# Optimization experiments

Hardware: AMD Instinct MI355X
Metric: run time of the kernel (lower is better)

The kernel has to match this reference:

```python
import jax, jax.numpy as jnp
import numpy as np

N = 100000        # nodes
E_RAND = 1500000  # random edges (plus N self-loops)
NFEAT = 64
NHID = 64
NHEADS = 8
ALPHA = 0.2       # leaky-relu slope


def setup_inputs() -> dict:
    key = jax.random.key(0)
    ks = jax.random.split(key, 10)
    x = jax.random.normal(ks[0], (N, NFEAT), jnp.float32)
    src = jax.random.randint(ks[1], (E_RAND,), 0, N)
    dst = jax.random.randint(ks[2], (E_RAND,), 0, N)
    loops = jnp.arange(N)
    edge_index = jnp.stack([jnp.concatenate([src, loops]),
                            jnp.concatenate([dst, loops])]).astype(jnp.int32)
    s = 0.1
    W_att = jax.random.normal(ks[3], (NHEADS, NFEAT, NHID), jnp.float32) * s
    a_att = jax.random.normal(ks[4], (NHEADS, 2 * NHID), jnp.float32) * s
    W_out = jax.random.normal(ks[5], (NHEADS * NHID, NFEAT), jnp.float32) * s
    a_out = jax.random.normal(ks[6], (2 * NFEAT,), jnp.float32) * s
    W1 = jax.random.normal(ks[7], (NFEAT, NFEAT * 10), jnp.float32) * s
    b1 = jnp.zeros((NFEAT * 10,), jnp.float32)
    W2 = jax.random.normal(ks[8], (NFEAT * 10, 10), jnp.float32) * s
    b2 = jnp.zeros((10,), jnp.float32)
    W3 = jax.random.normal(ks[9], (10, 1), jnp.float32) * s
    b3 = jnp.zeros((1,), jnp.float32)
    return dict(x=x, edge_index=edge_index, W_att=W_att, a_att=a_att,
                W_out=W_out, a_out=a_out, W1=W1, b1=b1, W2=W2, b2=b2,
                W3=W3, b3=b3)


def _gat_layer(x, row, col, W, a, concat):
    # x: [N,F], W: [F,D], a: [2D]. Faithful to pyGAT SpGraphAttentionLayer:
    # edge_e = exp(-leakyrelu(a . [h_src || h_dst])), normalized by rowsum.
    n = x.shape[0]
    h = x @ W                                   # [N, D]
    d = h.shape[1]
    alpha_src = h @ a[:d]                       # [N]
    alpha_dst = h @ a[d:]                       # [N]
    score = alpha_src[row] + alpha_dst[col]     # [E]
    edge_e = jnp.exp(-jax.nn.leaky_relu(score, ALPHA))   # [E]
    rowsum = jax.ops.segment_sum(edge_e, row, num_segments=n)            # [N]
    h_prime = jax.ops.segment_sum(edge_e[:, None] * h[col], row,
                                  num_segments=n)                        # [N, D]
    h_prime = h_prime / rowsum[:, None]
    return jax.nn.elu(h_prime) if concat else h_prime


def reference(x, edge_index, W_att, a_att, W_out, a_out, W1, b1, W2, b2, W3, b3):
    row, col = edge_index[0], edge_index[1]
    # multi-head attention, concat along features
    heads = jax.vmap(lambda W, a: _gat_layer(x, row, col, W, a, True))(W_att, a_att)  # [H,N,D]
    xh = jnp.transpose(heads, (1, 0, 2)).reshape(x.shape[0], -1)  # [N, H*D]
    xo = jax.nn.elu(_gat_layer(xh, row, col, W_out, a_out, False))  # [N, NFEAT]
    # dense MLP head
    z = jax.nn.relu(xo @ W1 + b1)
    z = jax.nn.relu(z @ W2 + b2)
    z = jax.nn.sigmoid(z @ W3 + b3)  # [N, 1]
    return z
```

## Files before the change

### kernel.cpp

```cpp
#include <hip/hip_runtime.h>
#include <hip/hip_bf16.h>
#include <math.h>

#define NF 64
#define NH 8
#define SLOPE 0.2f

typedef __hip_bfloat16 bf16;
typedef short short8 __attribute__((ext_vector_type(8)));
typedef unsigned int uint4v __attribute__((ext_vector_type(4)));
typedef float f32x4 __attribute__((ext_vector_type(4)));
typedef float f32x2 __attribute__((ext_vector_type(2)));

__device__ __forceinline__ float us2f(unsigned short u){
  union{ unsigned int i; float f; } c; c.i = ((unsigned int)u) << 16; return c.f;
}
__device__ __forceinline__ float lo16(unsigned int u){
  union{ unsigned int i; float f; } c; c.i = u << 16; return c.f;
}
__device__ __forceinline__ float hi16(unsigned int u){
  union{ unsigned int i; float f; } c; c.i = u & 0xFFFF0000u; return c.f;
}
__device__ __forceinline__ unsigned short f2b_rne(float v){
  union{ float f; unsigned int i; } c; c.f = v;
  unsigned int b = c.i + 0x7FFF + ((c.i >> 16) & 1);
  return (unsigned short)(b >> 16);
}
__device__ __forceinline__ f32x4 mfma16(short8 a, short8 b, f32x4 c){
  return __builtin_amdgcn_mfma_f32_16x16x32_bf16(a, b, c, 0, 0, 0);
}


__global__ void k_prep1(const float* __restrict__ Watt, const float* __restrict__ aatt,
                        short* __restrict__ Bp1){
  int f = blockIdx.x >> 1, ks = blockIdx.x & 1;
  int lane = threadIdx.x;
  int kg = lane >> 4, cl = lane & 15;
  int col = f * 16 + cl;
  for (int j = 0; j < 8; j++){
    int k = ks * 32 + kg * 8 + j;
    float val;
    if (col < 512){
      val = Watt[(size_t)(col >> 6) * 4096 + k * 64 + (col & 63)];
    } else {
      int h = (col - 512) & 7;
      const float* arow = aatt + h * 128 + ((col >= 520) ? 64 : 0);
      const float* wrow = Watt + (size_t)h * 4096 + k * 64;
      float s = 0.f;
      for (int d = 0; d < 64; d++) s += wrow[d] * arow[d];
      val = s;
    }
    unsigned short hu = f2b_rne(val);
    float lof = val - us2f(hu);
    Bp1[((size_t)(ks * 33) + f) * 512 + lane * 8 + j]       = (short)hu;
    Bp1[((size_t)((2 + ks) * 33) + f) * 512 + lane * 8 + j] = (short)f2b_rne(lof);
  }
}

__global__ void k_prep2(const float* __restrict__ Wout, const float* __restrict__ aout,
                        short* __restrict__ Bp2){
  int f = blockIdx.x >> 4, ks = blockIdx.x & 15;
  int lane = threadIdx.x;
  int kg = lane >> 4, cl = lane & 15;
  int col = f * 16 + cl;
  for (int j = 0; j < 8; j++){
    int k = ks * 32 + kg * 8 + j;
    float val = 0.f;
    if (col < 64){
      val = Wout[(size_t)k * 64 + col];
    } else if (col == 64 || col == 65){
      const float* arow = aout + ((col == 65) ? 64 : 0);
      const float* wrow = Wout + (size_t)k * 64;
      float s = 0.f;
      for (int d = 0; d < 64; d++) s += wrow[d] * arow[d];
      val = s;
    }
    unsigned short hu = f2b_rne(val);
    float lof = val - us2f(hu);
    Bp2[((size_t)(ks * 5) + f) * 512 + lane * 8 + j]        = (short)hu;
    Bp2[((size_t)((16 + ks) * 5) + f) * 512 + lane * 8 + j] = (short)f2b_rne(lof);
  }
}

__global__ void k_prep3(const float* __restrict__ W1, short* __restrict__ Bp3){
  int f = blockIdx.x >> 1, ks = blockIdx.x & 1;
  int lane = threadIdx.x;
  int kg = lane >> 4, cl = lane & 15;
  int col = f * 16 + cl;
  for (int j = 0; j < 8; j++){
    int k = ks * 32 + kg * 8 + j;
    float val = W1[(size_t)k * 640 + col];
    unsigned short hu = f2b_rne(val);
    float lof = val - us2f(hu);
    Bp3[((size_t)(ks * 40) + f) * 512 + lane * 8 + j]       = (short)hu;
    Bp3[((size_t)((2 + ks) * 40) + f) * 512 + lane * 8 + j] = (short)f2b_rne(lof);
  }
}

__global__ void k_prep4(const float* __restrict__ W2, short* __restrict__ Bp4){
  int ks = blockIdx.x;
  int lane = threadIdx.x;
  int kg = lane >> 4, cl = lane & 15;
  for (int j = 0; j < 8; j++){
    int k = ks * 32 + kg * 8 + j;
    float val = (cl < 10) ? W2[k * 10 + cl] : 0.f;
    unsigned short hu = f2b_rne(val);
    Bp4[((size_t)ks) * 512 + lane * 8 + j]        = (short)hu;
    Bp4[((size_t)(20 + ks)) * 512 + lane * 8 + j] = (short)f2b_rne(val - us2f(hu));
  }
}

__global__ void __launch_bounds__(256)
k_prep_x(const float* __restrict__ x, const short* __restrict__ Bp1,
         short* __restrict__ xb, float* __restrict__ a1s, float* __restrict__ a1d,
         int n_nodes){
  __shared__ short xsh[16][72];
  __shared__ short xsl[16][72];
  int n0 = blockIdx.x * 16;
  int t = threadIdx.x;
  for (int i = t; i < 16 * 64; i += 256){
    int r = i >> 6, c = i & 63;
    int nn = n0 + r;
    float v = (nn < n_nodes) ? x[(size_t)nn * NF + c] : 0.f;
    unsigned short hu = f2b_rne(v);
    float lof = v - us2f(hu);
    xsh[r][c] = (short)hu;
    xsl[r][c] = (short)f2b_rne(lof);
  }
  __syncthreads();
  for (int i = t; i < 16 * 8; i += 256){
    int r = i >> 3, c8 = (i & 7) * 8;
    int nn = n0 + r;
    if (nn < n_nodes)
      *reinterpret_cast<short8*>(xb + (size_t)nn * 64 + c8) =
        *reinterpret_cast<const short8*>(&xsh[r][c8]);
  }
  int wid = t >> 6, lane = t & 63;
  if (wid == 3){
    int rowa = lane & 15, kg = lane >> 4, cl = lane & 15;
    short8 ah[2], al[2];
    #pragma unroll
    for (int ks = 0; ks < 2; ks++){
      ah[ks] = *reinterpret_cast<const short8*>(&xsh[rowa][ks * 32 + kg * 8]);
      al[ks] = *reinterpret_cast<const short8*>(&xsl[rowa][ks * 32 + kg * 8]);
    }
    f32x4 acc = {0.f, 0.f, 0.f, 0.f};
    #pragma unroll
    for (int ks = 0; ks < 2; ks++){
      short8 b_h = *reinterpret_cast<const short8*>(Bp1 + ((size_t)(ks * 33) + 32) * 512 + lane * 8);
      short8 b_l = *reinterpret_cast<const short8*>(Bp1 + ((size_t)((2 + ks) * 33) + 32) * 512 + lane * 8);
      acc = mfma16(ah[ks], b_h, acc);
      acc = mfma16(al[ks], b_h, acc);
      acc = mfma16(ah[ks], b_l, acc);
    }
    #pragma unroll
    for (int reg = 0; reg < 4; reg++){
      int nn = n0 + kg * 4 + reg;
      if (nn < n_nodes){
        if (cl < 8) a1s[nn * NH + cl] = acc[reg];
        else        a1d[nn * NH + (cl - 8)] = acc[reg];
      }
    }
  }
}

__global__ void k_count(const int* __restrict__ row, int* __restrict__ cnt, int E){
  int e = blockIdx.x * blockDim.x + threadIdx.x;
  if (e < E) atomicAdd(&cnt[row[e]], 1);
}

__global__ void k_scan_a(const int* __restrict__ cnt, int* __restrict__ incl,
                         int* __restrict__ bsum, int n){
  __shared__ int s[1024];
  int i = blockIdx.x * 1024 + threadIdx.x;
  int v = (i < n) ? cnt[i] : 0;
  s[threadIdx.x] = v;
  __syncthreads();
  for (int d = 1; d < 1024; d <<= 1){
    int tv = (threadIdx.x >= d) ? s[threadIdx.x - d] : 0;
    __syncthreads();
    s[threadIdx.x] += tv;
    __syncthreads();
  }
  if (i < n) incl[i] = s[threadIdx.x];
  if (threadIdx.x == 1023) bsum[blockIdx.x] = s[1023];
}

__global__ void k_scan_b(const int* __restrict__ bsum, int* __restrict__ boff, int nb){
  __shared__ int s[128];
  int t = threadIdx.x;
  if (nb <= 128){
    int v = (t < nb) ? bsum[t] : 0;
    s[t] = v;
    __syncthreads();
    for (int d = 1; d < 128; d <<= 1){
      int tv = (t >= d) ? s[t - d] : 0;
      __syncthreads();
      s[t] += tv;
      __syncthreads();
    }
    if (t < nb) boff[t] = s[t] - v;
  } else if (t == 0){
    int run = 0;
    for (int b = 0; b < nb; b++){ boff[b] = run; run += bsum[b]; }
  }
}

__global__ void k_scan_c(const int* __restrict__ incl, const int* __restrict__ cnt,
                         const int* __restrict__ boff, int* __restrict__ rowptr,
                         int* __restrict__ wptr, int n){
  int i = blockIdx.x * 1024 + threadIdx.x;
  if (i < n){
    int start = incl[i] - cnt[i] + boff[blockIdx.x];
    rowptr[i] = start;
    wptr[i]   = start;
  }
}

__global__ void k_scatter(const int* __restrict__ row, const int* __restrict__ col,
                          int* __restrict__ wptr, int* __restrict__ scol, int E){
  int e = blockIdx.x * blockDim.x + threadIdx.x;
  if (e < E){
    int r = row[e];
    int pos = atomicAdd(&wptr[r], 1);
    scol[pos] = col[e];
  }
}

__global__ void __launch_bounds__(512, 2)
k_agg1_gemm2(const short* __restrict__ xb, const float* __restrict__ a1s,
             const float* __restrict__ a1d, const int* __restrict__ rowptr,
             const int* __restrict__ cnt, const int* __restrict__ scol,
             const short* __restrict__ Bp1, const short* __restrict__ Bp2,
             bf16* __restrict__ h2b, float* __restrict__ a2s,
             float* __restrict__ a2d, int n_nodes){
  __shared__ short Gh[8 * 600];
  __shared__ short xh[8][528];
  int n0   = blockIdx.x * 8;
  int wid  = threadIdx.x >> 6;
  int lane = threadIdx.x & 63;
  int h = lane >> 3, q = lane & 7;
  int n = n0 + wid;
  int gidx = wid * 600 + h * 72 + q * 8;

  if (n < n_nodes){
    float asrc = a1s[n * NH + h];
    int beg = rowptr[n], endk = beg + cnt[n];
    f32x2 acc2[4] = {{0.f,0.f},{0.f,0.f},{0.f,0.f},{0.f,0.f}};
    float rsum = 0.f;
    int k = beg;
    for (; k + 3 < endk; k += 4){
      int c0 = scol[k], c1 = scol[k + 1], c2 = scol[k + 2], c3 = scol[k + 3];
      uint4v x0 = *reinterpret_cast<const uint4v*>(xb + (size_t)c0 * 64 + q * 8);
      uint4v x1 = *reinterpret_cast<const uint4v*>(xb + (size_t)c1 * 64 + q * 8);
      uint4v x2 = *reinterpret_cast<const uint4v*>(xb + (size_t)c2 * 64 + q * 8);
      uint4v x3 = *reinterpret_cast<const uint4v*>(xb + (size_t)c3 * 64 + q * 8);
      float s0 = asrc + a1d[c0 * NH + h];
      float s1 = asrc + a1d[c1 * NH + h];
      float s2 = asrc + a1d[c2 * NH + h];
      float s3 = asrc + a1d[c3 * NH + h];
      float l0 = fmaxf(s0, SLOPE * s0);
      float l1 = fmaxf(s1, SLOPE * s1);
      float l2 = fmaxf(s2, SLOPE * s2);
      float l3 = fmaxf(s3, SLOPE * s3);
      float e0 = __expf(-l0);
      float e1 = __expf(-l1);
      float e2 = __expf(-l2);
      float e3 = __expf(-l3);
      rsum += (e0 + e1) + (e2 + e3);
      f32x2 ev0 = {e0, e0}, ev1 = {e1, e1}, ev2 = {e2, e2}, ev3 = {e3, e3};
      #pragma unroll
      for (int d = 0; d < 4; d++){
        f32x2 hv0 = {lo16(x0[d]), hi16(x0[d])};
        f32x2 hv1 = {lo16(x1[d]), hi16(x1[d])};
        f32x2 hv2 = {lo16(x2[d]), hi16(x2[d])};
        f32x2 hv3 = {lo16(x3[d]), hi16(x3[d])};
        acc2[d] += (ev0 * hv0 + ev1 * hv1) + (ev2 * hv2 + ev3 * hv3);
      }
    }
    for (; k < endk; ++k){
      int c0 = scol[k];
      uint4v x0 = *reinterpret_cast<const uint4v*>(xb + (size_t)c0 * 64 + q * 8);
      float s0 = asrc + a1d[c0 * NH + h];
      float l0 = fmaxf(s0, SLOPE * s0);
      float e0 = __expf(-l0);
      rsum += e0;
      f32x2 ev0 = {e0, e0};
      #pragma unroll
      for (int d = 0; d < 4; d++){
        f32x2 hv0 = {lo16(x0[d]), hi16(x0[d])};
        acc2[d] += ev0 * hv0;
      }
    }
    float inv = 1.f / rsum;
    short8 hv8;
    #pragma unroll
    for (int jj = 0; jj < 8; jj++)
      hv8[jj] = (short)f2b_rne(acc2[jj >> 1][jj & 1] * inv);
    *reinterpret_cast<short8*>(&Gh[gidx]) = hv8;
  } else {
    short8 z = {0,0,0,0,0,0,0,0};
    *reinterpret_cast<short8*>(&Gh[gidx]) = z;
  }
  __syncthreads();

  {
    int rowa = lane & 7;
    int kg   = lane >> 4, cl = lane & 15;
    short8 gah[2];
    #pragma unroll
    for (int ks = 0; ks < 2; ks++)
      gah[ks] = *reinterpret_cast<const short8*>(&Gh[rowa * 600 + wid * 72 + ks * 32 + kg * 8]);
    #pragma unroll
    for (int fc = 0; fc < 4; fc++){
      int f = wid * 4 + fc;
      f32x4 acc = {0.f, 0.f, 0.f, 0.f};
      #pragma unroll
      for (int ks = 0; ks < 2; ks++){
        short8 b_h = *reinterpret_cast<const short8*>(Bp1 + ((size_t)(ks * 33) + f) * 512 + lane * 8);
        short8 b_l = *reinterpret_cast<const short8*>(Bp1 + ((size_t)((2 + ks) * 33) + f) * 512 + lane * 8);
        acc = mfma16(gah[ks], b_h, acc);
        acc = mfma16(gah[ks], b_l, acc);
      }
      if (kg < 2){
        #pragma unroll
        for (int reg = 0; reg < 4; reg++){
          int r = kg * 4 + reg;
          float v = acc[reg];
          v = (v > 0.f) ? v : (__expf(v) - 1.f);
          xh[r][wid * 64 + fc * 16 + cl] = (short)f2b_rne(v);
        }
      }
    }
  }
  __syncthreads();

  if (wid < 5){
    int rowa = lane & 7;
    int kg   = lane >> 4;
    f32x4 acc = {0.f, 0.f, 0.f, 0.f};
    #pragma unroll 4
    for (int ks = 0; ks < 16; ks++){
      short8 a_h = *reinterpret_cast<const short8*>(&xh[rowa][ks * 32 + kg * 8]);
      short8 b_h = *reinterpret_cast<const short8*>(Bp2 + ((size_t)(ks * 5) + wid) * 512 + lane * 8);
      short8 b_l = *reinterpret_cast<const short8*>(Bp2 + ((size_t)((16 + ks) * 5) + wid) * 512 + lane * 8);
      acc = mfma16(a_h, b_h, acc);
      acc = mfma16(a_h, b_l, acc);
    }
    int cl = lane & 15;
    if (kg < 2){
      #pragma unroll
      for (int reg = 0; reg < 4; reg++){
        int nn = n0 + kg * 4 + reg;
        if (nn < n_nodes){
          if (wid < 4){
            h2b[(size_t)nn * 64 + wid * 16 + cl] = __float2bfloat16(acc[reg]);
          } else if (cl == 0){
            a2s[nn] = acc[reg];
          } else if (cl == 1){
            a2d[nn] = acc[reg];
          }
        }
      }
    }
  }
}

__global__ void __launch_bounds__(256)
k_agg2(const bf16* __restrict__ h2b, const float* __restrict__ a2s,
       const float* __restrict__ a2d, const int* __restrict__ rowptr,
       const int* __restrict__ cnt, const int* __restrict__ scol,
       float* __restrict__ xo, int n_nodes){
  int wid  = threadIdx.x >> 6;
  int lane = threadIdx.x & 63;
  int g = lane >> 3, sl = lane & 7;
  int n = blockIdx.x * 32 + wid * 8 + g;
  bool nv = (n < n_nodes);
  int beg = 0, deg = 0;
  float asrc = 0.f;
  if (nv){ beg = rowptr[n]; deg = cnt[n]; asrc = a2s[n]; }
  int mdeg = deg;
  #pragma unroll
  for (int m = 8; m < 64; m <<= 1){
    int o = __shfl_xor(mdeg, m);
    mdeg = (o > mdeg) ? o : mdeg;
  }
  f32x2 acc2[4] = {{0.f,0.f},{0.f,0.f},{0.f,0.f},{0.f,0.f}};
  float rsum = 0.f;
  int it = 0;
  for (; it + 1 < mdeg; it += 2){
    int i0 = (it     < deg) ? it     : 0;
    int i1 = (it + 1 < deg) ? it + 1 : 0;
    int c0 = scol[beg + i0];
    int c1 = scol[beg + i1];
    uint4v h0 = *reinterpret_cast<const uint4v*>(h2b + ((size_t)c0 << 6) + sl * 8);
    uint4v h1 = *reinterpret_cast<const uint4v*>(h2b + ((size_t)c1 << 6) + sl * 8);
    float s0 = asrc + a2d[c0];
    float s1 = asrc + a2d[c1];
    float l0 = fmaxf(s0, SLOPE * s0);
    float l1 = fmaxf(s1, SLOPE * s1);
    float e0 = __expf(-l0);
    float e1 = __expf(-l1);
    e0 = (it     < deg) ? e0 : 0.f;
    e1 = (it + 1 < deg) ? e1 : 0.f;
    rsum += e0 + e1;
    f32x2 ev0 = {e0, e0}, ev1 = {e1, e1};
    #pragma unroll
    for (int d = 0; d < 4; d++){
      f32x2 hv0 = {lo16(h0[d]), hi16(h0[d])};
      f32x2 hv1 = {lo16(h1[d]), hi16(h1[d])};
      acc2[d] += ev0 * hv0 + ev1 * hv1;
    }
  }
  if (it < mdeg){
    int i0 = (it < deg) ? it : 0;
    int c0 = scol[beg + i0];
    uint4v h0 = *reinterpret_cast<const uint4v*>(h2b + ((size_t)c0 << 6) + sl * 8);
    float s0 = asrc + a2d[c0];
    float l0 = fmaxf(s0, SLOPE * s0);
    float e0 = __expf(-l0);
    e0 = (it < deg) ? e0 : 0.f;
    rsum += e0;
    f32x2 ev0 = {e0, e0};
    #pragma unroll
    for (int d = 0; d < 4; d++){
      f32x2 hv0 = {lo16(h0[d]), hi16(h0[d])};
      acc2[d] += ev0 * hv0;
    }
  }
  if (nv){
    float inv = 1.f / rsum;
    float4 lo, hi;
    float vv[8];
    #pragma unroll
    for (int jj = 0; jj < 8; jj++){
      float v = acc2[jj >> 1][jj & 1] * inv;
      vv[jj] = (v > 0.f) ? v : (__expf(v) - 1.f);
    }
    lo.x = vv[0]; lo.y = vv[1]; lo.z = vv[2]; lo.w = vv[3];
    hi.x = vv[4]; hi.y = vv[5]; hi.z = vv[6]; hi.w = vv[7];
    *reinterpret_cast<float4*>(xo + (size_t)n * 64 + sl * 8)     = lo;
    *reinterpret_cast<float4*>(xo + (size_t)n * 64 + sl * 8 + 4) = hi;
  }
}

__global__ void __launch_bounds__(256)
k_mlp(const float* __restrict__ xo, const short* __restrict__ Bp3,
      const short* __restrict__ Bp4, const float* __restrict__ b1,
      const float* __restrict__ b2, const float* __restrict__ W3,
      const float* __restrict__ b3, float* __restrict__ out, int n_nodes){
  __shared__ short xsh[16][72];
  __shared__ short xsl[16][72];
  __shared__ short z1h[16][648];
  __shared__ float part[4][16][16];
  __shared__ float z2[16][10];
  int n0 = blockIdx.x * 16;
  int t  = threadIdx.x;
  for (int i = t; i < 16 * 64; i += 256){
    int r = i >> 6, c = i & 63;
    int nn = n0 + r;
    float v = (nn < n_nodes) ? xo[(size_t)nn * 64 + c] : 0.f;
    unsigned short hu = f2b_rne(v);
    float lof = v - us2f(hu);
    xsh[r][c] = (short)hu;
    xsl[r][c] = (short)f2b_rne(lof);
  }
  __syncthreads();
  int wid = t >> 6, lane = t & 63;
  int rowa = lane & 15, kg = lane >> 4, cl = lane & 15;
  {
    short8 ah[2], al[2];
    #pragma unroll
    for (int ks = 0; ks < 2; ks++){
      ah[ks] = *reinterpret_cast<const short8*>(&xsh[rowa][ks * 32 + kg * 8]);
      al[ks] = *reinterpret_cast<const short8*>(&xsl[rowa][ks * 32 + kg * 8]);
    }
    for (int f0 = 0; f0 < 10; f0++){
      int f = wid * 10 + f0;
      f32x4 acc = {0.f, 0.f, 0.f, 0.f};
      #pragma unroll
      for (int ks = 0; ks < 2; ks++){
        short8 b_h = *reinterpret_cast<const short8*>(Bp3 + ((size_t)(ks * 40) + f) * 512 + lane * 8);
        short8 b_l = *reinterpret_cast<const short8*>(Bp3 + ((size_t)((2 + ks) * 40) + f) * 512 + lane * 8);
        acc = mfma16(ah[ks], b_h, acc);
        acc = mfma16(al[ks], b_h, acc);
        acc = mfma16(ah[ks], b_l, acc);
      }
      int cc = f * 16 + cl;
      float bb = b1[cc];
      #pragma unroll
      for (int reg = 0; reg < 4; reg++)
        z1h[kg * 4 + reg][cc] = (short)f2b_rne(fmaxf(acc[reg] + bb, 0.f));
    }
  }
  __syncthreads();
  {
    f32x4 acc = {0.f, 0.f, 0.f, 0.f};
    #pragma unroll
    for (int kk = 0; kk < 5; kk++){
      int ks = wid * 5 + kk;
      short8 a_h = *reinterpret_cast<const short8*>(&z1h[rowa][ks * 32 + kg * 8]);
      short8 b_h = *reinterpret_cast<const short8*>(Bp4 + ((size_t)ks) * 512 + lane * 8);
      short8 b_l = *reinterpret_cast<const short8*>(Bp4 + ((size_t)(20 + ks)) * 512 + lane * 8);
      acc = mfma16(a_h, b_h, acc);
      acc = mfma16(a_h, b_l, acc);
    }
    #pragma unroll
    for (int reg = 0; reg < 4; reg++)
      part[wid][kg * 4 + reg][cl] = acc[reg];
  }
  __syncthreads();
  if (t < 160){
    int r = t / 10, c = t % 10;
    float v = (part[0][r][c] + part[1][r][c]) + (part[2][r][c] + part[3][r][c]);
    z2[r][c] = fmaxf(v + b2[c], 0.f);
  }
  __syncthreads();
  if (t < 16){
    int nn = n0 + t;
    if (nn < n_nodes){
      float acc = b3[0];
      #pragma unroll
      for (int kk = 0; kk < 10; kk++) acc += z2[t][kk] * W3[kk];
      out[nn] = 1.f / (1.f + __expf(-acc));
    }
  }
}

extern "C" void kernel_launch(void* const* d_in, const int* in_sizes, int n_in,
                              void* d_out, int out_size, void* d_ws, size_t ws_size,
                              hipStream_t stream){
  const float* x    = (const float*)d_in[0];
  const int*   ei   = (const int*)  d_in[1];
  const float* Watt = (const float*)d_in[2];
  const float* aatt = (const float*)d_in[3];
  const float* Wout = (const float*)d_in[4];
  const float* aout = (const float*)d_in[5];
  const float* W1   = (const float*)d_in[6];
  const float* b1   = (const float*)d_in[7];
  const float* W2   = (const float*)d_in[8];
  const float* b2   = (const float*)d_in[9];
  const float* W3   = (const float*)d_in[10];
  const float* b3   = (const float*)d_in[11];
  float* out = (float*)d_out;

  int N = in_sizes[0] / NF;
  int E = in_sizes[1] / 2;
  const int* row = ei;
  const int* col = ei + E;

  char* base = (char*)d_ws;
  size_t off = 0;
  auto alloc = [&](size_t bytes) -> void* {
    void* p = base + off;
    off = (off + bytes + 255) & ~(size_t)255;
    return p;
  };
  short* xb     = (short*)alloc((size_t)N * 64 * 2);
  bf16*  h2b    = (bf16*) alloc((size_t)N * 64 * 2);
  float* xo     = (float*)alloc((size_t)N * 64 * 4);
  float* a1s    = (float*)alloc((size_t)N * NH * 4);
  float* a1d    = (float*)alloc((size_t)N * NH * 4);
  float* a2s    = (float*)alloc((size_t)N * 4);
  float* a2d    = (float*)alloc((size_t)N * 4);
  int*   cnt    = (int*)  alloc((size_t)N * 4);
  int*   rowptr = (int*)  alloc((size_t)N * 4);
  int*   wptr   = (int*)  alloc((size_t)N * 4);
  int*   incl   = (int*)  alloc((size_t)N * 4);
  int    NB     = (N + 1023) / 1024;
  int*   bsum   = (int*)  alloc((size_t)NB * 4);
  int*   boff   = (int*)  alloc((size_t)NB * 4);
  int*   scol   = (int*)  alloc((size_t)E * 4);
  short* Bp1    = (short*)alloc((size_t)4 * 33 * 512 * 2);
  short* Bp2    = (short*)alloc((size_t)32 * 5 * 512 * 2);
  short* Bp3    = (short*)alloc((size_t)4 * 40 * 512 * 2);
  short* Bp4    = (short*)alloc((size_t)40 * 512 * 2);
  (void)ws_size; (void)n_in; (void)out_size;

  hipMemsetAsync(cnt, 0, (size_t)N * 4, stream);

  k_prep1     <<<66,              64, 0, stream>>>(Watt, aatt, Bp1);
  k_prep2     <<<80,              64, 0, stream>>>(Wout, aout, Bp2);
  k_prep3     <<<80,              64, 0, stream>>>(W1, Bp3);
  k_prep4     <<<20,              64, 0, stream>>>(W2, Bp4);
  k_prep_x    <<<(N + 15) / 16,  256, 0, stream>>>(x, Bp1, xb, a1s, a1d, N);
  k_count     <<<(E + 255) / 256, 256, 0, stream>>>(row, cnt, E);
  k_scan_a    <<<NB,             1024, 0, stream>>>(cnt, incl, bsum, N);
  k_scan_b    <<<1,               128, 0, stream>>>(bsum, boff, NB);
  k_scan_c    <<<NB,             1024, 0, stream>>>(incl, cnt, boff, rowptr, wptr, N);
  k_scatter   <<<(E + 255) / 256, 256, 0, stream>>>(row, col, wptr, scol, E);
  k_agg1_gemm2<<<(N + 7) / 8,     512, 0, stream>>>(xb, a1s, a1d, rowptr, cnt, scol,
                                                    Bp1, Bp2, h2b, a2s, a2d, N);
  k_agg2      <<<(N + 31) / 32,  256, 0, stream>>>(h2b, a2s, a2d, rowptr, cnt, scol, xo, N);
  k_mlp       <<<(N + 15) / 16,  256, 0, stream>>>(xo, Bp3, Bp4, b1, b2, W3, b3, out, N);
}
```

Measured before the change: 534.6 us.

## Compute first-layer edge aggregation with MFMA over 32-edge chunks

Replaces the per-lane scalar FMA edge aggregation in the fused agg1/gemm2 kernel with an MFMA formulation. Each wave handles 32 neighbours at a time: the attention weights for 8 heads become a bf16 B fragment, and gathered features form the A fragment. Partial row sums are then reduced with shuffles. This moves the aggregation arithmetic onto the matrix cores, at the cost of rounding edge weights to bf16, padding low-degree nodes to 32 edges, and doing scalar 2-byte gathers of features instead of 16-byte vector loads.

```diff
diff --git a/kernel.cpp b/kernel.cpp
--- a/kernel.cpp
+++ b/kernel.cpp
@@ -239,74 +239,72 @@
   int n0   = blockIdx.x * 8;
   int wid  = threadIdx.x >> 6;
   int lane = threadIdx.x & 63;
-  int h = lane >> 3, q = lane & 7;
+  int kg = lane >> 4, cl = lane & 15;
+  int hsel = lane & 7;
   int n = n0 + wid;
-  int gidx = wid * 600 + h * 72 + q * 8;
 
   if (n < n_nodes){
-    float asrc = a1s[n * NH + h];
-    int beg = rowptr[n], endk = beg + cnt[n];
-    f32x2 acc2[4] = {{0.f,0.f},{0.f,0.f},{0.f,0.f},{0.f,0.f}};
-    float rsum = 0.f;
-    int k = beg;
-    for (; k + 3 < endk; k += 4){
-      int c0 = scol[k], c1 = scol[k + 1], c2 = scol[k + 2], c3 = scol[k + 3];
-      uint4v x0 = *reinterpret_cast<const uint4v*>(xb + (size_t)c0 * 64 + q * 8);
-      uint4v x1 = *reinterpret_cast<const uint4v*>(xb + (size_t)c1 * 64 + q * 8);
-      uint4v x2 = *reinterpret_cast<const uint4v*>(xb + (size_t)c2 * 64 + q * 8);
-      uint4v x3 = *reinterpret_cast<const uint4v*>(xb + (size_t)c3 * 64 + q * 8);
-      float s0 = asrc + a1d[c0 * NH + h];
-      float s1 = asrc + a1d[c1 * NH + h];
-      float s2 = asrc + a1d[c2 * NH + h];
-      float s3 = asrc + a1d[c3 * NH + h];
-      float l0 = fmaxf(s0, SLOPE * s0);
-      float l1 = fmaxf(s1, SLOPE * s1);
-      float l2 = fmaxf(s2, SLOPE * s2);
-      float l3 = fmaxf(s3, SLOPE * s3);
-      float e0 = __expf(-l0);
-      float e1 = __expf(-l1);
-      float e2 = __expf(-l2);
-      float e3 = __expf(-l3);
-      rsum += (e0 + e1) + (e2 + e3);
-      f32x2 ev0 = {e0, e0}, ev1 = {e1, e1}, ev2 = {e2, e2}, ev3 = {e3, e3};
-      #pragma unroll
-      for (int d = 0; d < 4; d++){
-        f32x2 hv0 = {lo16(x0[d]), hi16(x0[d])};
-        f32x2 hv1 = {lo16(x1[d]), hi16(x1[d])};
-        f32x2 hv2 = {lo16(x2[d]), hi16(x2[d])};
-        f32x2 hv3 = {lo16(x3[d]), hi16(x3[d])};
-        acc2[d] += (ev0 * hv0 + ev1 * hv1) + (ev2 * hv2 + ev3 * hv3);
-      }
-    }
-    for (; k < endk; ++k){
-      int c0 = scol[k];
-      uint4v x0 = *reinterpret_cast<const uint4v*>(xb + (size_t)c0 * 64 + q * 8);
-      float s0 = asrc + a1d[c0 * NH + h];
-      float l0 = fmaxf(s0, SLOPE * s0);
-      float e0 = __expf(-l0);
-      rsum += e0;
-      f32x2 ev0 = {e0, e0};
-      #pragma unroll
-      for (int d = 0; d < 4; d++){
-        f32x2 hv0 = {lo16(x0[d]), hi16(x0[d])};
-        acc2[d] += ev0 * hv0;
-      }
-    }
+    int beg = rowptr[n], deg = cnt[n];
+    float asrc = a1s[n * NH + hsel];
+    f32x4 accD[4];
+    #pragma unroll
+    for (int fb = 0; fb < 4; fb++){ accD[fb][0]=0.f; accD[fb][1]=0.f; accD[fb][2]=0.f; accD[fb][3]=0.f; }
+    float rsum_part = 0.f;
+    for (int p = 0; p < deg; p += 32){
+      int c[8];
+      #pragma unroll
+      for (int j = 0; j < 8; j++){
+        int kk = p + kg * 8 + j;
+        c[j] = scol[beg + ((kk < deg) ? kk : 0)];
+      }
+      float ef[8];
+      #pragma unroll
+      for (int j = 0; j < 8; j++){
+        float s = asrc + a1d[c[j] * NH + hsel];
+        float l = fmaxf(s, SLOPE * s);
+        float e = __expf(-l);
+        ef[j] = ((p + kg * 8 + j) < deg) ? e : 0.f;
+        rsum_part += ef[j];
+      }
+      short8 bfrag;
+      #pragma unroll
+      for (int j = 0; j < 8; j++) bfrag[j] = (short)f2b_rne(ef[j]);
+      #pragma unroll
+      for (int fb = 0; fb < 4; fb++){
+        short8 afrag;
+        #pragma unroll
+        for (int j = 0; j < 8; j++)
+          afrag[j] = xb[c[j] * 64 + fb * 16 + cl];
+        accD[fb] = mfma16(afrag, bfrag, accD[fb]);
+      }
+    }
+    float rsum = rsum_part;
+    rsum += __shfl_xor(rsum, 16);
+    rsum += __shfl_xor(rsum, 32);
     float inv = 1.f / rsum;
-    short8 hv8;
-    #pragma unroll
-    for (int jj = 0; jj < 8; jj++)
-      hv8[jj] = (short)f2b_rne(acc2[jj >> 1][jj & 1] * inv);
-    *reinterpret_cast<short8*>(&Gh[gidx]) = hv8;
+    if (cl < 8){
+      #pragma unroll
+      for (int fb = 0; fb < 4; fb++){
+        #pragma unroll
+        for (int reg = 0; reg < 4; reg++)
+          Gh[wid * 600 + cl * 72 + fb * 16 + kg * 4 + reg] =
+            (short)f2b_rne(accD[fb][reg] * inv);
+      }
+    }
   } else {
-    short8 z = {0,0,0,0,0,0,0,0};
-    *reinterpret_cast<short8*>(&Gh[gidx]) = z;
+    if (cl < 8){
+      #pragma unroll
+      for (int fb = 0; fb < 4; fb++){
+        #pragma unroll
+        for (int reg = 0; reg < 4; reg++)
+          Gh[wid * 600 + cl * 72 + fb * 16 + kg * 4 + reg] = 0;
+      }
+    }
   }
   __syncthreads();
 
   {
     int rowa = lane & 7;
-    int kg   = lane >> 4, cl = lane & 15;
     short8 gah[2];
     #pragma unroll
     for (int ks = 0; ks < 2; ks++)
@@ -337,7 +335,6 @@
 
   if (wid < 5){
     int rowa = lane & 7;
-    int kg   = lane >> 4;
     f32x4 acc = {0.f, 0.f, 0.f, 0.f};
     #pragma unroll 4
     for (int ks = 0; ks < 16; ks++){
@@ -347,7 +344,6 @@
       acc = mfma16(a_h, b_h, acc);
       acc = mfma16(a_h, b_l, acc);
     }
-    int cl = lane & 15;
     if (kg < 2){
       #pragma unroll
       for (int reg = 0; reg < 4; reg++){
```

Measured after the change: 522.6 us. 1.02x faster.
